# Optimization experiments

Hardware: AMD Instinct MI355X
Metric: run time of the kernel (lower is better)

The kernel has to match this reference:

```python
import jax, jax.numpy as jnp
import numpy as np

D_MODEL = 1024
D_STATE = 16
D_CONV = 4
EXPAND = 2
MLP_EXPAND = 2
D_INNER = EXPAND * D_MODEL          # 2048
DT_RANK = (D_MODEL + 15) // 16      # 64
BATCH, SEQ = 2, 1024


def setup_inputs() -> dict:
    key = jax.random.key(0)
    ks = jax.random.split(key, 16)
    s = 0.02
    inp = {
        "x": jax.random.normal(ks[0], (BATCH, SEQ, D_MODEL), jnp.float32),
        "norm1_g": jnp.ones((D_MODEL,), jnp.float32),
        "norm1_b": jnp.zeros((D_MODEL,), jnp.float32),
        "in_proj_w": jax.random.normal(ks[1], (2 * D_INNER, D_MODEL), jnp.float32) * s,
        "conv_w": jax.random.normal(ks[2], (D_INNER, 1, D_CONV), jnp.float32) * s,
        "conv_b": jnp.zeros((D_INNER,), jnp.float32),
        "x_proj_w": jax.random.normal(ks[3], (DT_RANK + 2 * D_STATE, D_INNER), jnp.float32) * s,
        "dt_proj_w": jax.random.normal(ks[4], (D_INNER, DT_RANK), jnp.float32) * s,
        "dt_proj_b": jax.random.normal(ks[5], (D_INNER,), jnp.float32) * 0.1,
        "A_log": jnp.log(jnp.broadcast_to(jnp.arange(1, D_STATE + 1, dtype=jnp.float32), (D_INNER, D_STATE))),
        "D_param": jnp.ones((D_INNER,), jnp.float32),
        "out_proj_w": jax.random.normal(ks[6], (D_MODEL, D_INNER), jnp.float32) * s,
        "norm2_g": jnp.ones((D_MODEL,), jnp.float32),
        "norm2_b": jnp.zeros((D_MODEL,), jnp.float32),
        "mlp_w1": jax.random.normal(ks[7], (MLP_EXPAND * D_MODEL, D_MODEL), jnp.float32) * s,
        "mlp_b1": jnp.zeros((MLP_EXPAND * D_MODEL,), jnp.float32),
        "mlp_w2": jax.random.normal(ks[8], (D_MODEL, MLP_EXPAND * D_MODEL), jnp.float32) * s,
        "mlp_b2": jnp.zeros((D_MODEL,), jnp.float32),
    }
    return inp


def _layernorm(x, g, b, eps=1e-5):
    m = jnp.mean(x, axis=-1, keepdims=True)
    v = jnp.var(x, axis=-1, keepdims=True)
    return (x - m) * jax.lax.rsqrt(v + eps) * g + b


def _silu(x):
    return x * jax.nn.sigmoid(x)


def _mamba(x, in_proj_w, conv_w, conv_b, x_proj_w, dt_proj_w, dt_proj_b, A_log, D_param, out_proj_w):
    # x: (B, L, d_model)
    xz = x @ in_proj_w.T                              # (B, L, 2*Di)
    xc, z = jnp.split(xz, 2, axis=-1)                 # each (B, L, Di)
    # causal depthwise conv over time
    xc_t = xc.transpose(0, 2, 1)                      # (B, Di, L)
    xc_t = jax.lax.conv_general_dilated(
        xc_t, conv_w, window_strides=(1,), padding=[(D_CONV - 1, 0)],
        dimension_numbers=("NCH", "OIH", "NCH"), feature_group_count=D_INNER,
    ) + conv_b[None, :, None]
    xc = _silu(xc_t).transpose(0, 2, 1)               # (B, L, Di)

    dbc = xc @ x_proj_w.T                             # (B, L, dt_rank + 2N)
    dt, Bm, Cm = jnp.split(dbc, [DT_RANK, DT_RANK + D_STATE], axis=-1)
    dt = jax.nn.softplus(dt @ dt_proj_w.T + dt_proj_b)  # (B, L, Di)
    A = -jnp.exp(A_log)                               # (Di, N)

    def step(h, inp):
        dt_t, B_t, C_t, x_t = inp                     # (B,Di),(B,N),(B,N),(B,Di)
        dA = jnp.exp(dt_t[..., None] * A)             # (B, Di, N)
        h = dA * h + (dt_t * x_t)[..., None] * B_t[:, None, :]
        y = jnp.einsum("bdn,bn->bd", h, C_t)
        return h, y

    h0 = jnp.zeros((x.shape[0], D_INNER, D_STATE), x.dtype)
    xs = (dt.transpose(1, 0, 2), Bm.transpose(1, 0, 2), Cm.transpose(1, 0, 2), xc.transpose(1, 0, 2))
    _, ys = jax.lax.scan(step, h0, xs)                # ys: (L, B, Di)
    y = ys.transpose(1, 0, 2) + xc * D_param          # skip term D*x
    y = y * _silu(z)
    return y @ out_proj_w.T                           # (B, L, d_model)


def reference(x, norm1_g, norm1_b, in_proj_w, conv_w, conv_b, x_proj_w, dt_proj_w,
              dt_proj_b, A_log, D_param, out_proj_w, norm2_g, norm2_b,
              mlp_w1, mlp_b1, mlp_w2, mlp_b2):
    # residual + Mamba(LN(x))  (droppath=0 -> identity)
    h = x + _mamba(_layernorm(x, norm1_g, norm1_b), in_proj_w, conv_w, conv_b,
                   x_proj_w, dt_proj_w, dt_proj_b, A_log, D_param, out_proj_w)
    # residual + MLP(LN(h))    (dropout eval -> identity)
    m = _layernorm(h, norm2_g, norm2_b)
    m = jax.nn.gelu(m @ mlp_w1.T + mlp_b1, approximate=False) @ mlp_w2.T + mlp_b2
    return h + m
```

## Files before the change

kernel.cpp:

```cpp
#include <hip/hip_runtime.h>
#include <math.h>

#define D_MODEL 1024
#define D_INNER 2048
#define DT_RANK 64
#define D_STATE 16
#define NBC 96
#define BATCH 2
#define SEQ 1024
#define TOK (BATCH*SEQ)
#define CS 32
#define NCH 32
#define XKSPLIT 16

typedef __attribute__((ext_vector_type(8))) short short8;
typedef __attribute__((ext_vector_type(4))) float f32x4;
typedef __attribute__((ext_vector_type(4))) unsigned short us4;

__device__ __forceinline__ float softplus_f(float x) {
    return (x > 20.0f) ? x : log1pf(__expf(x));
}
__device__ __forceinline__ float gelu_f(float x) {
    return 0.5f * x * (1.0f + erff(x * 0.70710678118654752f));
}
__device__ __forceinline__ float silu_f(float x) {
    return x / (1.0f + __expf(-x));
}
__device__ __forceinline__ ushort f2bf(float f) {
    unsigned u = __float_as_uint(f);
    unsigned r = (u + 0x7fffu + ((u >> 16) & 1u)) >> 16;
    return (ushort)r;
}
__device__ __forceinline__ float bf2f(ushort u) {
    return __uint_as_float(((unsigned)u) << 16);
}

__global__ void convert_weights_kernel(const float* __restrict__ Wp, const float* __restrict__ Wo,
                                       const float* __restrict__ W1, const float* __restrict__ W2,
                                       const float* __restrict__ Wx, const float* __restrict__ Wdt,
                                       ushort* __restrict__ Wpb, ushort* __restrict__ Wob,
                                       ushort* __restrict__ W1b, ushort* __restrict__ W2b,
                                       ushort* __restrict__ Wxb, ushort* __restrict__ Wdtb) {
    int i = blockIdx.x * 256 + threadIdx.x;
    const float* src; ushort* dst; int off;
    if      (i < 1048576) { src = Wp;  dst = Wpb;  off = i; }
    else if (i < 1572864) { src = Wo;  dst = Wob;  off = i - 1048576; }
    else if (i < 2097152) { src = W1;  dst = W1b;  off = i - 1572864; }
    else if (i < 2621440) { src = W2;  dst = W2b;  off = i - 2097152; }
    else if (i < 2670592) { src = Wx;  dst = Wxb;  off = i - 2621440; }
    else if (i < 2703360) { src = Wdt; dst = Wdtb; off = i - 2670592; }
    else return;
    float4 v = ((const float4*)src)[off];
    ushort4 o;
    o.x = f2bf(v.x); o.y = f2bf(v.y); o.z = f2bf(v.z); o.w = f2bf(v.w);
    ((ushort4*)dst)[off] = o;
}

__global__ void ln_bf16_kernel(const float* __restrict__ x, const float* __restrict__ g,
                               const float* __restrict__ b, ushort* __restrict__ out) {
    int row = blockIdx.x;
    const float* xr = x + (size_t)row * D_MODEL;
    ushort* outr = out + (size_t)row * D_MODEL;
    int tid = threadIdx.x;
    float4 v = ((const float4*)xr)[tid];
    float s  = v.x + v.y + v.z + v.w;
    float sq = v.x*v.x + v.y*v.y + v.z*v.z + v.w*v.w;
    #pragma unroll
    for (int o = 32; o > 0; o >>= 1) {
        s  += __shfl_down(s,  o);
        sq += __shfl_down(sq, o);
    }
    __shared__ float ss[4], ssq[4];
    int wid = tid >> 6, lane = tid & 63;
    if (lane == 0) { ss[wid] = s; ssq[wid] = sq; }
    __syncthreads();
    if (tid == 0) {
        float a = 0.f, c = 0.f;
        for (int i = 0; i < 4; i++) { a += ss[i]; c += ssq[i]; }
        ss[0] = a; ssq[0] = c;
    }
    __syncthreads();
    float mean = ss[0] * (1.0f / D_MODEL);
    float var  = ssq[0] * (1.0f / D_MODEL) - mean * mean;
    float rstd = rsqrtf(var + 1e-5f);
    float4 gg = ((const float4*)g)[tid];
    float4 bb = ((const float4*)b)[tid];
    ushort4 o;
    o.x = f2bf((v.x - mean) * rstd * gg.x + bb.x);
    o.y = f2bf((v.y - mean) * rstd * gg.y + bb.y);
    o.z = f2bf((v.z - mean) * rstd * gg.z + bb.z);
    o.w = f2bf((v.w - mean) * rstd * gg.w + bb.w);
    ((ushort4*)outr)[tid] = o;
}

template<int BM, int BN, int ACT, bool BIAS, bool RES, bool OUTBF>
__global__ __launch_bounds__(256)
void mfma_gemm(const ushort* __restrict__ A, const ushort* __restrict__ W,
               const float* __restrict__ bias,
               const float* __restrict__ res, int ldr,
               void* __restrict__ Cout, int ldc, int K) {
    constexpr int WM = BM / 2, WN = BN / 2, FM = WM / 16, FN = WN / 16;
    __shared__ __align__(16) ushort As[2][BM * 32];
    __shared__ __align__(16) ushort Ws[2][BN * 32];
    const int tid  = threadIdx.x;
    const int lane = tid & 63, w = tid >> 6;
    const int wr = w >> 1, wc = w & 1;
    const int row0 = blockIdx.y * BM, col0 = blockIdx.x * BN;
    const int l16 = lane >> 4, l15 = lane & 15;
    const int srow = tid >> 2;
    const int scol = (tid & 3) * 8;
    const int nk = K / 32;

    f32x4 acc[FM][FN] = {};

    auto stage = [&](int kk, int buf) {
        const int k0 = kk * 32;
        #pragma unroll
        for (int s = 0; s < BM / 64; s++) {
            const ushort* g = A + (size_t)(row0 + s * 64 + srow) * K + k0 + scol;
            __builtin_amdgcn_global_load_lds(
                (const __attribute__((address_space(1))) void*)g,
                (__attribute__((address_space(3))) void*)((char*)&As[buf][0] + s * 4096 + w * 1024),
                16, 0, 0);
        }
        #pragma unroll
        for (int s = 0; s < BN / 64; s++) {
            const ushort* g = W + (size_t)(col0 + s * 64 + srow) * K + k0 + scol;
            __builtin_amdgcn_global_load_lds(
                (const __attribute__((address_space(1))) void*)g,
                (__attribute__((address_space(3))) void*)((char*)&Ws[buf][0] + s * 4096 + w * 1024),
                16, 0, 0);
        }
    };

    stage(0, 0);
    __syncthreads();

    for (int kk = 0; kk < nk; kk++) {
        const int cur = kk & 1;
        if (kk + 1 < nk) stage(kk + 1, cur ^ 1);

        short8 a[FM], b[FN];
        #pragma unroll
        for (int m = 0; m < FM; m++)
            a[m] = *(const short8*)(&As[cur][0] + (wr * WM + m * 16 + l15) * 32 + l16 * 8);
        #pragma unroll
        for (int n = 0; n < FN; n++)
            b[n] = *(const short8*)(&Ws[cur][0] + (wc * WN + n * 16 + l15) * 32 + l16 * 8);
        #pragma unroll
        for (int m = 0; m < FM; m++)
            #pragma unroll
            for (int n = 0; n < FN; n++)
                acc[m][n] = __builtin_amdgcn_mfma_f32_16x16x32_bf16(a[m], b[n], acc[m][n], 0, 0, 0);
        __syncthreads();
    }

    #pragma unroll
    for (int m = 0; m < FM; m++) {
        const int r0 = row0 + wr * WM + m * 16 + l16 * 4;
        #pragma unroll
        for (int n = 0; n < FN; n++) {
            const int c = col0 + wc * WN + n * 16 + l15;
            const float bv = BIAS ? bias[c] : 0.f;
            #pragma unroll
            for (int q = 0; q < 4; q++) {
                const int r = r0 + q;
                float v = acc[m][n][q] + bv;
                if (ACT == 1) v = softplus_f(v);
                else if (ACT == 2) v = gelu_f(v);
                if (RES) v += res[(size_t)r * ldr + c];
                if (OUTBF) ((ushort*)Cout)[(size_t)r * ldc + c] = f2bf(v);
                else       ((float*)Cout)[(size_t)r * ldc + c] = v;
            }
        }
    }
}

__global__ __launch_bounds__(256)
void xproj_split_kernel(const ushort* __restrict__ A,
                        const ushort* __restrict__ W,
                        float* __restrict__ part) {
    __shared__ __align__(16) ushort As[2][128 * 64];
    __shared__ __align__(16) ushort Bs[2][96 * 64];
    const int tid = threadIdx.x;
    const int lane = tid & 63, w = tid >> 6;
    const int l16 = lane >> 4, l15 = lane & 15;
    const int kbase = blockIdx.x * (D_INNER / XKSPLIT);
    const int row0 = blockIdx.y * 128;
    const int srow = tid >> 3;
    const int scol = (tid & 7) * 8;

    f32x4 acc[2][6] = {};

    auto stage = [&](int k0, int buf) {
        #pragma unroll
        for (int s = 0; s < 4; s++) {
            const ushort* g = A + (size_t)(row0 + s * 32 + srow) * D_INNER + kbase + k0 + scol;
            __builtin_amdgcn_global_load_lds(
                (const __attribute__((address_space(1))) void*)g,
                (__attribute__((address_space(3))) void*)((char*)&As[buf][0] + s * 4096 + w * 1024),
                16, 0, 0);
        }
        #pragma unroll
        for (int s = 0; s < 3; s++) {
            const ushort* g = W + (size_t)(s * 32 + srow) * D_INNER + kbase + k0 + scol;
            __builtin_amdgcn_global_load_lds(
                (const __attribute__((address_space(1))) void*)g,
                (__attribute__((address_space(3))) void*)((char*)&Bs[buf][0] + s * 4096 + w * 1024),
                16, 0, 0);
        }
    };

    stage(0, 0);
    __syncthreads();

    const int nk = (D_INNER / XKSPLIT) / 64;
    for (int kk = 0; kk < nk; kk++) {
        const int cur = kk & 1;
        if (kk + 1 < nk) stage((kk + 1) * 64, cur ^ 1);
        #pragma unroll
        for (int ks = 0; ks < 2; ks++) {
            short8 a[2], b[6];
            #pragma unroll
            for (int m = 0; m < 2; m++)
                a[m] = *(const short8*)(&As[cur][0] + (w * 32 + m * 16 + l15) * 64 + ks * 32 + l16 * 8);
            #pragma unroll
            for (int n = 0; n < 6; n++)
                b[n] = *(const short8*)(&Bs[cur][0] + (n * 16 + l15) * 64 + ks * 32 + l16 * 8);
            #pragma unroll
            for (int m = 0; m < 2; m++)
                #pragma unroll
                for (int n = 0; n < 6; n++)
                    acc[m][n] = __builtin_amdgcn_mfma_f32_16x16x32_bf16(a[m], b[n], acc[m][n], 0, 0, 0);
        }
        __syncthreads();
    }

    float* p = part + (size_t)blockIdx.x * D_INNER * NBC;
    #pragma unroll
    for (int m = 0; m < 2; m++) {
        const int r0 = row0 + w * 32 + m * 16 + l16 * 4;
        #pragma unroll
        for (int n = 0; n < 6; n++) {
            const int c = n * 16 + l15;
            #pragma unroll
            for (int q = 0; q < 4; q++)
                p[(size_t)(r0 + q) * NBC + c] = acc[m][n][q];
        }
    }
}

__global__ void xproj_reduce_kernel(const float* __restrict__ part,
                                    float* __restrict__ dbc, ushort* __restrict__ dtin_b) {
    int i = blockIdx.x * 256 + threadIdx.x;
    if (i >= D_INNER * NBC) return;
    float s = 0.f;
    #pragma unroll
    for (int k = 0; k < XKSPLIT; k++) s += part[(size_t)k * D_INNER * NBC + i];
    dbc[i] = s;
    int r = i / NBC, c = i - r * NBC;
    if (c < DT_RANK) dtin_b[r * DT_RANK + c] = f2bf(s);
}

__global__ void conv_silu_kernel(const ushort* __restrict__ xzb, const float* __restrict__ cw,
                                 const float* __restrict__ cb, ushort* __restrict__ xcb) {
    int idx = blockIdx.x * 256 + threadIdx.x;
    int c  = idx & (D_INNER - 1);
    int bt = idx >> 11;
    int b  = bt >> 10;
    int t  = bt & (SEQ - 1);
    float acc = cb[c];
    #pragma unroll
    for (int j = 0; j < 4; j++) {
        int tt = t - 3 + j;
        if (tt >= 0) acc += cw[c*4 + j] * bf2f(xzb[((size_t)(b*SEQ + tt)) * 4096 + c]);
    }
    xcb[idx] = f2bf(silu_f(acc));
}

__global__ __launch_bounds__(256)
void scan_chunk_kernel(const ushort* __restrict__ dtb, const float* __restrict__ dbc,
                       const ushort* __restrict__ xcb, const float* __restrict__ A_log,
                       float* __restrict__ chunkA, float* __restrict__ chunkH) {
    __shared__ ushort dtS[64][36];
    __shared__ ushort xS[64][36];
    __shared__ float  BS[16][36];
    const int bid = blockIdx.x;
    const int dg = bid & 31, cc = (bid >> 5) & 31, b = bid >> 10;
    const int d0 = dg * 64;
    const int tid = threadIdx.x, lane = tid & 63, wv = tid >> 6;
    const int rbase = b * SEQ + cc * CS;

    #pragma unroll
    for (int k = 0; k < 8; k++) {
        int tt = k * 4 + wv;
        size_t row = (size_t)(rbase + tt);
        dtS[lane][tt] = dtb[row * D_INNER + d0 + lane];
        xS[lane][tt]  = xcb[row * D_INNER + d0 + lane];
    }
    #pragma unroll
    for (int k = 0; k < 2; k++) {
        int ii = k * 256 + tid;
        int val = ii & 15, tt = ii >> 4;
        BS[val][tt] = dbc[(size_t)(rbase + tt) * NBC + DT_RANK + val];
    }
    __syncthreads();

    const int d_local = tid >> 2, ng = tid & 3, nb = ng * 4;
    const int d = d0 + d_local;
    float Arow[4];
    #pragma unroll
    for (int j = 0; j < 4; j++) Arow[j] = -__expf(A_log[d * D_STATE + nb + j]);
    float h[4] = {};
    float ap[4] = {1.f, 1.f, 1.f, 1.f};
    #pragma unroll
    for (int it = 0; it < 8; ++it) {
        us4 dtu = *(const us4*)&dtS[d_local][it * 4];
        us4 xu  = *(const us4*)&xS[d_local][it * 4];
        f32x4 Bv[4];
        #pragma unroll
        for (int j = 0; j < 4; j++) Bv[j] = *(const f32x4*)&BS[nb + j][it * 4];
        #pragma unroll
        for (int q = 0; q < 4; ++q) {
            float dtv = bf2f(dtu[q]);
            float dtx = dtv * bf2f(xu[q]);
            #pragma unroll
            for (int j = 0; j < 4; j++) {
                float dA = __expf(dtv * Arow[j]);
                ap[j] *= dA;
                h[j] = dA * h[j] + dtx * Bv[j][q];
            }
        }
    }
    size_t obase = ((size_t)((b * NCH + cc) * D_STATE) + nb) * D_INNER + d;
    #pragma unroll
    for (int j = 0; j < 4; j++) {
        chunkA[obase + (size_t)j * D_INNER] = ap[j];
        chunkH[obase + (size_t)j * D_INNER] = h[j];
    }
}

__global__ void scan_combine_kernel(const float* __restrict__ chunkA, float* __restrict__ chunkH) {
    int idx = blockIdx.x * 256 + threadIdx.x;
    int d = idx & (D_INNER - 1);
    int r = idx >> 11;
    int n = r & (D_STATE - 1);
    int b = r >> 4;
    float h = 0.f;
    for (int c = 0; c < NCH; c++) {
        size_t o = ((size_t)((b * NCH + c) * D_STATE + n)) * D_INNER + d;
        float a  = chunkA[o];
        float hl = chunkH[o];
        chunkH[o] = h;
        h = a * h + hl;
    }
}

__global__ __launch_bounds__(256)
void scan_final_kernel(const ushort* __restrict__ dtb, const float* __restrict__ dbc,
                       const ushort* __restrict__ xcb, const float* __restrict__ A_log,
                       const float* __restrict__ chunkH, const ushort* __restrict__ xzb,
                       const float* __restrict__ Dp, ushort* __restrict__ yb) {
    __shared__ ushort dtS[64][36];
    __shared__ ushort xS[64][36];
    __shared__ ushort zS[64][36];
    __shared__ float  BS[16][36];
    __shared__ float  CSld[16][36];
    __shared__ ushort ySt[64][36];
    const int bid = blockIdx.x;
    const int dg = bid & 31, cc = (bid >> 5) & 31, b = bid >> 10;
    const int d0 = dg * 64;
    const int tid = threadIdx.x, lane = tid & 63, wv = tid >> 6;
    const int rbase = b * SEQ + cc * CS;

    #pragma unroll
    for (int k = 0; k < 8; k++) {
        int tt = k * 4 + wv;
        size_t row = (size_t)(rbase + tt);
        dtS[lane][tt] = dtb[row * D_INNER + d0 + lane];
        xS[lane][tt]  = xcb[row * D_INNER + d0 + lane];
        zS[lane][tt]  = xzb[row * 4096 + 2048 + d0 + lane];
    }
    #pragma unroll
    for (int k = 0; k < 4; k++) {
        int ii = k * 256 + tid;
        int val = ii & 31, tt = ii >> 5;
        float v = dbc[(size_t)(rbase + tt) * NBC + DT_RANK + val];
        if (val < 16) BS[val][tt] = v;
        else          CSld[val - 16][tt] = v;
    }
    __syncthreads();

    const int d_local = tid >> 2, ng = tid & 3, nb = ng * 4;
    const int d = d0 + d_local;
    float Arow[4];
    #pragma unroll
    for (int j = 0; j < 4; j++) Arow[j] = -__expf(A_log[d * D_STATE + nb + j]);
    float h[4];
    size_t obase = ((size_t)((b * NCH + cc) * D_STATE) + nb) * D_INNER + d;
    #pragma unroll
    for (int j = 0; j < 4; j++) h[j] = chunkH[obase + (size_t)j * D_INNER];
    const float Dpv = Dp[d];

    #pragma unroll
    for (int it = 0; it < 8; ++it) {
        us4 dtu = *(const us4*)&dtS[d_local][it * 4];
        us4 xu  = *(const us4*)&xS[d_local][it * 4];
        f32x4 Bv[4], Cv[4];
        #pragma unroll
        for (int j = 0; j < 4; j++) {
            Bv[j] = *(const f32x4*)&BS[nb + j][it * 4];
            Cv[j] = *(const f32x4*)&CSld[nb + j][it * 4];
        }
        float yv4[4];
        #pragma unroll
        for (int q = 0; q < 4; ++q) {
            float dtv = bf2f(dtu[q]);
            float dtx = dtv * bf2f(xu[q]);
            float yv = 0.f;
            #pragma unroll
            for (int j = 0; j < 4; j++) {
                float dA = __expf(dtv * Arow[j]);
                h[j] = dA * h[j] + dtx * Bv[j][q];
                yv += h[j] * Cv[j][q];
            }
            yv4[q] = yv;
        }
        #pragma unroll
        for (int q = 0; q < 4; ++q) {
            yv4[q] += __shfl_xor(yv4[q], 1);
            yv4[q] += __shfl_xor(yv4[q], 2);
        }
        if (ng == 0) {
            us4 zu = *(const us4*)&zS[d_local][it * 4];
            us4 xo = *(const us4*)&xS[d_local][it * 4];
            us4 o;
            #pragma unroll
            for (int q = 0; q < 4; ++q) {
                float z = bf2f(zu[q]);
                o[q] = f2bf((yv4[q] + bf2f(xo[q]) * Dpv) * silu_f(z));
            }
            *(us4*)&ySt[d_local][it * 4] = o;
        }
    }
    __syncthreads();
    #pragma unroll
    for (int k = 0; k < 8; k++) {
        int tt = k * 4 + wv;
        yb[(size_t)(rbase + tt) * D_INNER + d0 + lane] = ySt[lane][tt];
    }
}

extern "C" void kernel_launch(void* const* d_in, const int* in_sizes, int n_in,
                              void* d_out, int out_size, void* d_ws, size_t ws_size,
                              hipStream_t stream) {
    const float* x    = (const float*)d_in[0];
    const float* n1g  = (const float*)d_in[1];
    const float* n1b  = (const float*)d_in[2];
    const float* Wp   = (const float*)d_in[3];
    const float* cw   = (const float*)d_in[4];
    const float* cb   = (const float*)d_in[5];
    const float* Wx   = (const float*)d_in[6];
    const float* Wdt  = (const float*)d_in[7];
    const float* bdt  = (const float*)d_in[8];
    const float* Alog = (const float*)d_in[9];
    const float* Dp   = (const float*)d_in[10];
    const float* Wo   = (const float*)d_in[11];
    const float* n2g  = (const float*)d_in[12];
    const float* n2b  = (const float*)d_in[13];
    const float* W1   = (const float*)d_in[14];
    const float* b1   = (const float*)d_in[15];
    const float* W2   = (const float*)d_in[16];
    const float* b2   = (const float*)d_in[17];
    float* out = (float*)d_out;
    float* ws  = (float*)d_ws;

    const size_t M1 = 1024 * 1024;
    ushort* xzb   = (ushort*)ws;
    ushort* xcb   = (ushort*)(ws + 8*M1);
    ushort* dtb_b = (ushort*)(ws + 10*M1);
    float*  part  = ws + 14*M1;
    float*  hbuf  = ws + 14*M1;
    float*  dbc   = ws + 18*M1;
    ushort* dtin_b= (ushort*)(ws + 18*M1 + 262144);
    ushort* xnb   = (ushort*)(ws + 18*M1 + 524288);
    ushort* mb    = xnb;
    ushort* yb    = (ushort*)(ws + 20*M1);
    ushort* t1b   = yb;
    ushort* Wpb   = (ushort*)(ws + 22*M1);
    float*  chunkA= ws + 22*M1;
    ushort* Wob   = (ushort*)(ws + 24*M1);
    ushort* W1b   = (ushort*)(ws + 25*M1);
    ushort* W2b   = (ushort*)(ws + 26*M1);
    ushort* Wxb   = (ushort*)(ws + 27*M1);
    ushort* Wdtb  = (ushort*)(ws + 27*M1 + 131072);
    float*  chunkH = out;

    convert_weights_kernel<<<(2703360 + 255)/256, 256, 0, stream>>>(
        Wp, Wo, W1, W2, Wx, Wdt, Wpb, Wob, W1b, W2b, Wxb, Wdtb);

    ln_bf16_kernel<<<TOK, 256, 0, stream>>>(x, n1g, n1b, xnb);
    mfma_gemm<128,128,0,false,false,true><<<dim3(4096/128, 2048/128), 256, 0, stream>>>(
        xnb, Wpb, nullptr, nullptr, 0, xzb, 2*D_INNER, D_MODEL);
    conv_silu_kernel<<<TOK*D_INNER/256, 256, 0, stream>>>(xzb, cw, cb, xcb);
    xproj_split_kernel<<<dim3(XKSPLIT, 2048/128), 256, 0, stream>>>(xcb, Wxb, part);
    xproj_reduce_kernel<<<(D_INNER*NBC + 255)/256, 256, 0, stream>>>(part, dbc, dtin_b);
    mfma_gemm<128,128,1,true,false,true><<<dim3(2048/128, 2048/128), 256, 0, stream>>>(
        dtin_b, Wdtb, bdt, nullptr, 0, dtb_b, D_INNER, DT_RANK);
    scan_chunk_kernel<<<BATCH*NCH*(D_INNER/64), 256, 0, stream>>>(dtb_b, dbc, xcb, Alog, chunkA, chunkH);
    scan_combine_kernel<<<BATCH*D_STATE*D_INNER/256, 256, 0, stream>>>(chunkA, chunkH);
    scan_final_kernel<<<BATCH*NCH*(D_INNER/64), 256, 0, stream>>>(dtb_b, dbc, xcb, Alog, chunkH,
                                                                  xzb, Dp, yb);
    mfma_gemm<128,64,0,false,true,false><<<dim3(1024/64, 2048/128), 256, 0, stream>>>(
        yb, Wob, nullptr, x, D_MODEL, hbuf, D_MODEL, D_INNER);
    ln_bf16_kernel<<<TOK, 256, 0, stream>>>(hbuf, n2g, n2b, mb);
    mfma_gemm<128,128,2,true,false,true><<<dim3(2048/128, 2048/128), 256, 0, stream>>>(
        mb, W1b, b1, nullptr, 0, t1b, D_INNER, D_MODEL);
    mfma_gemm<128,64,0,true,true,false><<<dim3(1024/64, 2048/128), 256, 0, stream>>>(
        t1b, W2b, b2, hbuf, D_MODEL, out, D_MODEL, D_INNER);
}
```

Baseline: 257.3 us.

## Fuse LN1 with weight conversion, fold scan combine into final, shrink GEMM tiles

```diff
diff --git a/kernel.cpp b/kernel.cpp
--- a/kernel.cpp
+++ b/kernel.cpp
@@ -35,13 +35,51 @@
     return __uint_as_float(((unsigned)u) << 16);
 }
 
-__global__ void convert_weights_kernel(const float* __restrict__ Wp, const float* __restrict__ Wo,
-                                       const float* __restrict__ W1, const float* __restrict__ W2,
-                                       const float* __restrict__ Wx, const float* __restrict__ Wdt,
-                                       ushort* __restrict__ Wpb, ushort* __restrict__ Wob,
-                                       ushort* __restrict__ W1b, ushort* __restrict__ W2b,
-                                       ushort* __restrict__ Wxb, ushort* __restrict__ Wdtb) {
-    int i = blockIdx.x * 256 + threadIdx.x;
+__global__ void prep_kernel(const float* __restrict__ x, const float* __restrict__ g,
+                            const float* __restrict__ b, ushort* __restrict__ ln_out,
+                            const float* __restrict__ Wp, const float* __restrict__ Wo,
+                            const float* __restrict__ W1, const float* __restrict__ W2,
+                            const float* __restrict__ Wx, const float* __restrict__ Wdt,
+                            ushort* __restrict__ Wpb, ushort* __restrict__ Wob,
+                            ushort* __restrict__ W1b, ushort* __restrict__ W2b,
+                            ushort* __restrict__ Wxb, ushort* __restrict__ Wdtb) {
+    int tid = threadIdx.x;
+    if (blockIdx.x < TOK) {
+        int row = blockIdx.x;
+        const float* xr = x + (size_t)row * D_MODEL;
+        ushort* outr = ln_out + (size_t)row * D_MODEL;
+        float4 v = ((const float4*)xr)[tid];
+        float s  = v.x + v.y + v.z + v.w;
+        float sq = v.x*v.x + v.y*v.y + v.z*v.z + v.w*v.w;
+        #pragma unroll
+        for (int o = 32; o > 0; o >>= 1) {
+            s  += __shfl_down(s,  o);
+            sq += __shfl_down(sq, o);
+        }
+        __shared__ float ss[4], ssq[4];
+        int wid = tid >> 6, lane = tid & 63;
+        if (lane == 0) { ss[wid] = s; ssq[wid] = sq; }
+        __syncthreads();
+        if (tid == 0) {
+            float a = 0.f, c = 0.f;
+            for (int i = 0; i < 4; i++) { a += ss[i]; c += ssq[i]; }
+            ss[0] = a; ssq[0] = c;
+        }
+        __syncthreads();
+        float mean = ss[0] * (1.0f / D_MODEL);
+        float var  = ssq[0] * (1.0f / D_MODEL) - mean * mean;
+        float rstd = rsqrtf(var + 1e-5f);
+        float4 gg = ((const float4*)g)[tid];
+        float4 bb = ((const float4*)b)[tid];
+        ushort4 o;
+        o.x = f2bf((v.x - mean) * rstd * gg.x + bb.x);
+        o.y = f2bf((v.y - mean) * rstd * gg.y + bb.y);
+        o.z = f2bf((v.z - mean) * rstd * gg.z + bb.z);
+        o.w = f2bf((v.w - mean) * rstd * gg.w + bb.w);
+        ((ushort4*)outr)[tid] = o;
+        return;
+    }
+    int i = (blockIdx.x - TOK) * 256 + tid;
     const float* src; ushort* dst; int off;
     if      (i < 1048576) { src = Wp;  dst = Wpb;  off = i; }
     else if (i < 1572864) { src = Wo;  dst = Wob;  off = i - 1048576; }
@@ -332,34 +370,19 @@
             }
         }
     }
-    size_t obase = ((size_t)((b * NCH + cc) * D_STATE) + nb) * D_INNER + d;
-    #pragma unroll
-    for (int j = 0; j < 4; j++) {
-        chunkA[obase + (size_t)j * D_INNER] = ap[j];
-        chunkH[obase + (size_t)j * D_INNER] = h[j];
-    }
-}
-
-__global__ void scan_combine_kernel(const float* __restrict__ chunkA, float* __restrict__ chunkH) {
-    int idx = blockIdx.x * 256 + threadIdx.x;
-    int d = idx & (D_INNER - 1);
-    int r = idx >> 11;
-    int n = r & (D_STATE - 1);
-    int b = r >> 4;
-    float h = 0.f;
-    for (int c = 0; c < NCH; c++) {
-        size_t o = ((size_t)((b * NCH + c) * D_STATE + n)) * D_INNER + d;
-        float a  = chunkA[o];
-        float hl = chunkH[o];
-        chunkH[o] = h;
-        h = a * h + hl;
-    }
+    size_t obase = ((size_t)((b * NCH + cc) * D_INNER) + d) * D_STATE + nb;
+    f32x4 av, hv;
+    #pragma unroll
+    for (int j = 0; j < 4; j++) { av[j] = ap[j]; hv[j] = h[j]; }
+    *(f32x4*)&chunkA[obase] = av;
+    *(f32x4*)&chunkH[obase] = hv;
 }
 
 __global__ __launch_bounds__(256)
 void scan_final_kernel(const ushort* __restrict__ dtb, const float* __restrict__ dbc,
                        const ushort* __restrict__ xcb, const float* __restrict__ A_log,
-                       const float* __restrict__ chunkH, const ushort* __restrict__ xzb,
+                       const float* __restrict__ chunkA, const float* __restrict__ chunkH,
+                       const ushort* __restrict__ xzb,
                        const float* __restrict__ Dp, ushort* __restrict__ yb) {
     __shared__ ushort dtS[64][36];
     __shared__ ushort xS[64][36];
@@ -389,18 +412,26 @@
         if (val < 16) BS[val][tt] = v;
         else          CSld[val - 16][tt] = v;
     }
-    __syncthreads();
 
     const int d_local = tid >> 2, ng = tid & 3, nb = ng * 4;
     const int d = d0 + d_local;
+
+    f32x4 hv = {0.f, 0.f, 0.f, 0.f};
+    #pragma unroll 4
+    for (int c = 0; c < cc; ++c) {
+        size_t off = ((size_t)((b * NCH + c) * D_INNER) + d) * D_STATE + nb;
+        f32x4 a  = *(const f32x4*)&chunkA[off];
+        f32x4 hl = *(const f32x4*)&chunkH[off];
+        hv = a * hv + hl;
+    }
     float Arow[4];
     #pragma unroll
     for (int j = 0; j < 4; j++) Arow[j] = -__expf(A_log[d * D_STATE + nb + j]);
     float h[4];
-    size_t obase = ((size_t)((b * NCH + cc) * D_STATE) + nb) * D_INNER + d;
-    #pragma unroll
-    for (int j = 0; j < 4; j++) h[j] = chunkH[obase + (size_t)j * D_INNER];
+    #pragma unroll
+    for (int j = 0; j < 4; j++) h[j] = hv[j];
     const float Dpv = Dp[d];
+    __syncthreads();
 
     #pragma unroll
     for (int it = 0; it < 8; ++it) {
@@ -496,26 +527,24 @@
     ushort* Wdtb  = (ushort*)(ws + 27*M1 + 131072);
     float*  chunkH = out;
 
-    convert_weights_kernel<<<(2703360 + 255)/256, 256, 0, stream>>>(
-        Wp, Wo, W1, W2, Wx, Wdt, Wpb, Wob, W1b, W2b, Wxb, Wdtb);
-
-    ln_bf16_kernel<<<TOK, 256, 0, stream>>>(x, n1g, n1b, xnb);
+    prep_kernel<<<TOK + (2703360 + 255)/256, 256, 0, stream>>>(
+        x, n1g, n1b, xnb, Wp, Wo, W1, W2, Wx, Wdt, Wpb, Wob, W1b, W2b, Wxb, Wdtb);
+
     mfma_gemm<128,128,0,false,false,true><<<dim3(4096/128, 2048/128), 256, 0, stream>>>(
         xnb, Wpb, nullptr, nullptr, 0, xzb, 2*D_INNER, D_MODEL);
     conv_silu_kernel<<<TOK*D_INNER/256, 256, 0, stream>>>(xzb, cw, cb, xcb);
     xproj_split_kernel<<<dim3(XKSPLIT, 2048/128), 256, 0, stream>>>(xcb, Wxb, part);
     xproj_reduce_kernel<<<(D_INNER*NBC + 255)/256, 256, 0, stream>>>(part, dbc, dtin_b);
-    mfma_gemm<128,128,1,true,false,true><<<dim3(2048/128, 2048/128), 256, 0, stream>>>(
+    mfma_gemm<64,128,1,true,false,true><<<dim3(2048/128, 2048/64), 256, 0, stream>>>(
         dtin_b, Wdtb, bdt, nullptr, 0, dtb_b, D_INNER, DT_RANK);
     scan_chunk_kernel<<<BATCH*NCH*(D_INNER/64), 256, 0, stream>>>(dtb_b, dbc, xcb, Alog, chunkA, chunkH);
-    scan_combine_kernel<<<BATCH*D_STATE*D_INNER/256, 256, 0, stream>>>(chunkA, chunkH);
-    scan_final_kernel<<<BATCH*NCH*(D_INNER/64), 256, 0, stream>>>(dtb_b, dbc, xcb, Alog, chunkH,
-                                                                  xzb, Dp, yb);
-    mfma_gemm<128,64,0,false,true,false><<<dim3(1024/64, 2048/128), 256, 0, stream>>>(
+    scan_final_kernel<<<BATCH*NCH*(D_INNER/64), 256, 0, stream>>>(dtb_b, dbc, xcb, Alog,
+                                                                  chunkA, chunkH, xzb, Dp, yb);
+    mfma_gemm<64,64,0,false,true,false><<<dim3(1024/64, 2048/64), 256, 0, stream>>>(
         yb, Wob, nullptr, x, D_MODEL, hbuf, D_MODEL, D_INNER);
     ln_bf16_kernel<<<TOK, 256, 0, stream>>>(hbuf, n2g, n2b, mb);
-    mfma_gemm<128,128,2,true,false,true><<<dim3(2048/128, 2048/128), 256, 0, stream>>>(
+    mfma_gemm<64,128,2,true,false,true><<<dim3(2048/128, 2048/64), 256, 0, stream>>>(
         mb, W1b, b1, nullptr, 0, t1b, D_INNER, D_MODEL);
-    mfma_gemm<128,64,0,true,true,false><<<dim3(1024/64, 2048/128), 256, 0, stream>>>(
+    mfma_gemm<64,64,0,true,true,false><<<dim3(1024/64, 2048/64), 256, 0, stream>>>(
         t1b, W2b, b2, hbuf, D_MODEL, out, D_MODEL, D_INNER);
 }
```

Measured after the change: 225.2 us. -12.5%, faster.
